# Optimization experiments

Measured on AMD Instinct MI355X. Metric: run time of the kernel, lower is better.

## Reference

```python
import jax, jax.numpy as jnp
import numpy as np

T = 16777216            # flat replay-buffer length (timesteps)
DISCOUNT = 0.99         # gamma
FINAL_REWARD = 0.0      # bootstrap value for the last timestep
TERM_PROB = 0.001       # ~1000-step episodes


def setup_inputs() -> dict:
    key = jax.random.key(0)
    k1, k2 = jax.random.split(key)
    reward = jax.random.normal(k1, (T,), dtype=jnp.float32)
    terminal = jax.random.bernoulli(k2, TERM_PROB, (T,))
    return {"terminal": terminal, "reward": reward}


def _discounted_cumret(terminal, reward):
    # Reverse-time linear recurrence (same math as tf.scan over reversed seq):
    #   c_t = r_t                      if terminal_t
    #   c_t = r_t + discount * c_{t+1} otherwise
    # i.e. c_t = a_t * c_{t+1} + b_t with a_t = discount*(1-term_t), b_t = r_t.
    # Expressed as a (log-depth) associative scan over the reversed sequence.
    a = jnp.where(terminal, jnp.zeros((), reward.dtype),
                  jnp.asarray(DISCOUNT, reward.dtype))
    a_rev = a[::-1]
    b_rev = reward[::-1]
    # fold the initializer (final_reward) into the first reversed element
    b_rev = b_rev.at[0].add(a_rev[0] * jnp.asarray(FINAL_REWARD, reward.dtype))

    def combine(e1, e2):
        # composition of affine maps x -> a*x + b (e1 applied first)
        a1, b1 = e1
        a2, b2 = e2
        return a1 * a2, a2 * b1 + b2

    _, y_rev = jax.lax.associative_scan(combine, (a_rev, b_rev))
    return y_rev[::-1]


def reference(terminal, reward):
    return _discounted_cumret(terminal, reward)
```

## Files before the change

### kernel.cpp

```cpp
#include <hip/hip_runtime.h>


constexpr int   TPB  = 256;
constexpr int   IPT  = 32;
constexpr int   TILE = TPB * IPT;
constexpr float DISC = 0.99f;
constexpr float L2DISC = -0.0144995696f;

__device__ __forceinline__ void wave_suffix_scan(float& A, float& B, int lane) {
    #pragma unroll
    for (int off = 1; off < 64; off <<= 1) {
        float oA = __shfl_down(A, off, 64);
        float oB = __shfl_down(B, off, 64);
        if (lane + off < 64) { B = A * oB + B; A = A * oA; }
    }
}

__global__ __launch_bounds__(TPB) void k_local(
        const int* __restrict__ term, const float* __restrict__ rew,
        float* __restrict__ out, float2* __restrict__ agg,
        int* __restrict__ lastT, long long T) {
    __shared__ float2 sWA[TPB / 64];
    __shared__ int    sLast[TPB / 64];

    const int t = threadIdx.x;
    const int lane = t & 63, wav = t >> 6;
    const int b = blockIdx.x;
    const long long lo   = (long long)b * TILE;
    const long long base = lo + (long long)t * IPT;
    const bool fast = (base + IPT <= T);

    float r[IPT];
    unsigned mask = 0;
    if (fast) {
        const float4* rp = (const float4*)(rew + base);
        const int4*   tp = (const int4*)(term + base);
        #pragma unroll
        for (int q = 0; q < IPT / 4; ++q) {
            float4 rv = rp[q];
            int4   tv = tp[q];
            r[4*q+0] = rv.x; r[4*q+1] = rv.y; r[4*q+2] = rv.z; r[4*q+3] = rv.w;
            mask |= (tv.x ? 1u : 0u) << (4*q+0);
            mask |= (tv.y ? 1u : 0u) << (4*q+1);
            mask |= (tv.z ? 1u : 0u) << (4*q+2);
            mask |= (tv.w ? 1u : 0u) << (4*q+3);
        }
    } else {
        #pragma unroll
        for (int k = 0; k < IPT; ++k) {
            long long i = base + k;
            if (i < T) { r[k] = rew[i]; mask |= (term[i] ? 1u : 0u) << k; }
            else       { r[k] = 0.f; }
        }
    }

    float A = 1.f, B = 0.f;
    #pragma unroll
    for (int k = IPT - 1; k >= 0; --k) {
        float ak = ((mask >> k) & 1u) ? 0.f : DISC;
        if (!fast && base + k >= T) ak = 1.f;
        B = ak * B + r[k]; A = ak * A;
    }

    float IA = A, IB = B;
    wave_suffix_scan(IA, IB, lane);

    int myLast = mask ? (int)(base + (31 - __clz(mask))) : -1;
    #pragma unroll
    for (int off = 32; off > 0; off >>= 1)
        myLast = max(myLast, __shfl_down(myLast, off, 64));

    if (lane == 0) { sWA[wav] = make_float2(IA, IB); sLast[wav] = myLast; }
    __syncthreads();

    if (t == 0) {
        float2 g = sWA[0];
        int lt = sLast[0];
        #pragma unroll
        for (int w = 1; w < TPB / 64; ++w) {
            float2 h = sWA[w];
            g.y = g.x * h.y + g.y; g.x = g.x * h.x;
            lt = max(lt, sLast[w]);
        }
        agg[b] = g;
        lastT[b] = max(lt, (int)lo - 1);
    }

    float EWA = 1.f, EWB = 0.f;
    #pragma unroll
    for (int w = 0; w < TPB / 64; ++w)
        if (w > wav) { float2 h = sWA[w]; EWB = EWA*h.y + EWB; EWA = EWA*h.x; }

    float EA = __shfl_down(IA, 1, 64);
    float EB = __shfl_down(IB, 1, 64);
    if (lane == 63) { EA = 1.f; EB = 0.f; }

    float y = EA * EWB + EB;

    #pragma unroll
    for (int k = IPT - 1; k >= 0; --k) {
        float ak = ((mask >> k) & 1u) ? 0.f : DISC;
        if (!fast && base + k >= T) ak = 1.f;
        y = ak * y + r[k]; r[k] = y;
    }

    if (fast) {
        float4* op = (float4*)(out + base);
        #pragma unroll
        for (int q = 0; q < IPT / 4; ++q)
            op[q] = make_float4(r[4*q+0], r[4*q+1], r[4*q+2], r[4*q+3]);
    } else {
        #pragma unroll
        for (int k = 0; k < IPT; ++k) {
            long long i = base + k;
            if (i < T) out[i] = r[k];
        }
    }
}

__global__ __launch_bounds__(TPB) void k_fix(
        const float2* __restrict__ agg, const int* __restrict__ lastT,
        float* __restrict__ out, int numBlocks, long long T) {
    __shared__ float2 sWB[TPB / 64];

    const int t = threadIdx.x;
    const int lane = t & 63, wav = t >> 6;
    const int b = blockIdx.x;

    const int cpt = (numBlocks + TPB - 1) / TPB;
    float VA = 1.f, VB = 0.f;
    #pragma unroll
    for (int k = cpt - 1; k >= 0; --k) {
        int g = t * cpt + k;
        if (g > b && g < numBlocks) {
            float2 q = agg[g];
            VB = q.x * VB + q.y; VA = q.x * VA;
        }
    }
    wave_suffix_scan(VA, VB, lane);
    if (lane == 0) sWB[wav] = make_float2(VA, VB);
    __syncthreads();

    float FA = sWB[0].x, FB = sWB[0].y;
    #pragma unroll
    for (int w = 1; w < TPB / 64; ++w) {
        float2 h = sWB[w];
        FB = FA * h.y + FB; FA = FA * h.x;
    }
    const float yin = FB;
    if (yin == 0.f) return;

    const long long lo = (long long)b * TILE;
    const long long hi = min(lo + TILE, T) - 1;
    const long long start = (long long)lastT[b] + 1;

    for (long long i = start + t; i <= hi; i += TPB) {
        float d = (float)(int)(hi + 1 - i);
        out[i] += exp2f(d * L2DISC) * yin;
    }
}

extern "C" void kernel_launch(void* const* d_in, const int* in_sizes, int n_in,
                              void* d_out, int out_size, void* d_ws, size_t ws_size,
                              hipStream_t stream) {
    const int*   term = (const int*)d_in[0];
    const float* rew  = (const float*)d_in[1];
    float*       out  = (float*)d_out;

    const long long T = (long long)in_sizes[1];
    const int numBlocks = (int)((T + TILE - 1) / TILE);

    float2* agg   = (float2*)d_ws;
    int*    lastT = (int*)(agg + numBlocks);

    k_local<<<numBlocks, TPB, 0, stream>>>(term, rew, out, agg, lastT, T);
    k_fix  <<<numBlocks, TPB, 0, stream>>>(agg, lastT, out, numBlocks, T);
}
```

Measured before the change: 183.3 us.

## Split block tile into register-prefetched chunks scanned back-to-front with carry

Each thread now handles four chunks of 8 elements instead of one run of 32. The block walks the chunks from last to first, carrying the running affine aggregate between them, and double-buffers the next chunk's loads in registers. The goal is to cut per-thread register use (32 floats down to 8) and get coalesced, chunk-contiguous memory access while overlapping loads with the scan. The cost is four block-wide scans and two barriers per chunk where there used to be one scan per tile.

After: 178.6 us. -2.6%, faster.

```diff
diff --git a/kernel.cpp b/kernel.cpp
--- a/kernel.cpp
+++ b/kernel.cpp
@@ -1,10 +1,12 @@
 #include <hip/hip_runtime.h>
 
 
-constexpr int   TPB  = 256;
-constexpr int   IPT  = 32;
-constexpr int   TILE = TPB * IPT;
-constexpr float DISC = 0.99f;
+constexpr int   TPB   = 256;
+constexpr int   IPTC  = 8;
+constexpr int   NCH   = 4;
+constexpr int   CHUNK = TPB * IPTC;
+constexpr int   TILE  = CHUNK * NCH;
+constexpr float DISC  = 0.99f;
 constexpr float L2DISC = -0.0144995696f;
 
 __device__ __forceinline__ void wave_suffix_scan(float& A, float& B, int lane) {
@@ -26,95 +28,182 @@
     const int t = threadIdx.x;
     const int lane = t & 63, wav = t >> 6;
     const int b = blockIdx.x;
-    const long long lo   = (long long)b * TILE;
-    const long long base = lo + (long long)t * IPT;
-    const bool fast = (base + IPT <= T);
-
-    float r[IPT];
-    unsigned mask = 0;
-    if (fast) {
-        const float4* rp = (const float4*)(rew + base);
-        const int4*   tp = (const int4*)(term + base);
+    const long long lo = (long long)b * TILE;
+    const bool fastblk = (lo + TILE <= T);
+
+    float At = 1.f, Bt = 0.f;
+    int   lt = -1;
+
+    if (fastblk) {
+        float4 bR[2][IPTC / 4];
+        int4   bT[2][IPTC / 4];
+
+        {
+            const long long base = lo + (long long)(NCH - 1) * CHUNK
+                                      + (long long)t * IPTC;
+            const float4* rp = (const float4*)(rew + base);
+            const int4*   tp = (const int4*)(term + base);
+            #pragma unroll
+            for (int q = 0; q < IPTC / 4; ++q) {
+                bR[(NCH - 1) & 1][q] = rp[q];
+                bT[(NCH - 1) & 1][q] = tp[q];
+            }
+        }
+
         #pragma unroll
-        for (int q = 0; q < IPT / 4; ++q) {
-            float4 rv = rp[q];
-            int4   tv = tp[q];
-            r[4*q+0] = rv.x; r[4*q+1] = rv.y; r[4*q+2] = rv.z; r[4*q+3] = rv.w;
-            mask |= (tv.x ? 1u : 0u) << (4*q+0);
-            mask |= (tv.y ? 1u : 0u) << (4*q+1);
-            mask |= (tv.z ? 1u : 0u) << (4*q+2);
-            mask |= (tv.w ? 1u : 0u) << (4*q+3);
+        for (int c = NCH - 1; c >= 0; --c) {
+            if (c > 0) {
+                const long long nbase = lo + (long long)(c - 1) * CHUNK
+                                           + (long long)t * IPTC;
+                const float4* rp = (const float4*)(rew + nbase);
+                const int4*   tp = (const int4*)(term + nbase);
+                #pragma unroll
+                for (int q = 0; q < IPTC / 4; ++q) {
+                    bR[(c - 1) & 1][q] = rp[q];
+                    bT[(c - 1) & 1][q] = tp[q];
+                }
+            }
+            const int p = c & 1;
+            const long long base = lo + (long long)c * CHUNK + (long long)t * IPTC;
+
+            float r[IPTC];
+            unsigned mask = 0;
+            #pragma unroll
+            for (int q = 0; q < IPTC / 4; ++q) {
+                float4 rv = bR[p][q];
+                int4   tv = bT[p][q];
+                r[4*q+0] = rv.x; r[4*q+1] = rv.y; r[4*q+2] = rv.z; r[4*q+3] = rv.w;
+                mask |= (tv.x ? 1u : 0u) << (4*q+0);
+                mask |= (tv.y ? 1u : 0u) << (4*q+1);
+                mask |= (tv.z ? 1u : 0u) << (4*q+2);
+                mask |= (tv.w ? 1u : 0u) << (4*q+3);
+            }
+
+            float A = 1.f, B = 0.f;
+            #pragma unroll
+            for (int k = IPTC - 1; k >= 0; --k) {
+                float ak = ((mask >> k) & 1u) ? 0.f : DISC;
+                B = ak * B + r[k]; A = ak * A;
+            }
+
+            float IA = A, IB = B;
+            wave_suffix_scan(IA, IB, lane);
+
+            int myLast = mask ? (int)(base + (31 - __clz(mask))) : -1;
+            #pragma unroll
+            for (int off = 32; off > 0; off >>= 1)
+                myLast = max(myLast, __shfl_down(myLast, off, 64));
+
+            if (lane == 0) { sWA[wav] = make_float2(IA, IB); sLast[wav] = myLast; }
+            __syncthreads();
+
+            float2 g = sWA[0];
+            int cl = sLast[0];
+            #pragma unroll
+            for (int w = 1; w < TPB / 64; ++w) {
+                float2 h = sWA[w];
+                g.y = g.x * h.y + g.y; g.x = g.x * h.x;
+                cl = max(cl, sLast[w]);
+            }
+            float EWA = 1.f, EWB = 0.f;
+            #pragma unroll
+            for (int w = 0; w < TPB / 64; ++w)
+                if (w > wav) { float2 h = sWA[w]; EWB = EWA*h.y + EWB; EWA = EWA*h.x; }
+
+            float EA = __shfl_down(IA, 1, 64);
+            float EB = __shfl_down(IB, 1, 64);
+            if (lane == 63) { EA = 1.f; EB = 0.f; }
+
+            const float Yc = Bt;
+            float y = EA * (EWA * Yc + EWB) + EB;
+
+            #pragma unroll
+            for (int k = IPTC - 1; k >= 0; --k) {
+                float ak = ((mask >> k) & 1u) ? 0.f : DISC;
+                y = ak * y + r[k]; r[k] = y;
+            }
+
+            float4* op = (float4*)(out + base);
+            #pragma unroll
+            for (int q = 0; q < IPTC / 4; ++q)
+                op[q] = make_float4(r[4*q+0], r[4*q+1], r[4*q+2], r[4*q+3]);
+
+            Bt = g.x * Bt + g.y;
+            At = g.x * At;
+            lt = max(lt, cl);
+            __syncthreads();
         }
     } else {
-        #pragma unroll
-        for (int k = 0; k < IPT; ++k) {
-            long long i = base + k;
-            if (i < T) { r[k] = rew[i]; mask |= (term[i] ? 1u : 0u) << k; }
-            else       { r[k] = 0.f; }
-        }
-    }
-
-    float A = 1.f, B = 0.f;
-    #pragma unroll
-    for (int k = IPT - 1; k >= 0; --k) {
-        float ak = ((mask >> k) & 1u) ? 0.f : DISC;
-        if (!fast && base + k >= T) ak = 1.f;
-        B = ak * B + r[k]; A = ak * A;
-    }
-
-    float IA = A, IB = B;
-    wave_suffix_scan(IA, IB, lane);
-
-    int myLast = mask ? (int)(base + (31 - __clz(mask))) : -1;
-    #pragma unroll
-    for (int off = 32; off > 0; off >>= 1)
-        myLast = max(myLast, __shfl_down(myLast, off, 64));
-
-    if (lane == 0) { sWA[wav] = make_float2(IA, IB); sLast[wav] = myLast; }
-    __syncthreads();
+        for (int c = NCH - 1; c >= 0; --c) {
+            const long long base = lo + (long long)c * CHUNK + (long long)t * IPTC;
+            float r[IPTC];
+            unsigned mask = 0;
+            #pragma unroll
+            for (int k = 0; k < IPTC; ++k) {
+                long long i = base + k;
+                if (i < T) { r[k] = rew[i]; mask |= (term[i] ? 1u : 0u) << k; }
+                else       { r[k] = 0.f; }
+            }
+            float A = 1.f, B = 0.f;
+            #pragma unroll
+            for (int k = IPTC - 1; k >= 0; --k) {
+                float ak = ((mask >> k) & 1u) ? 0.f : DISC;
+                if (base + k >= T) ak = 1.f;
+                B = ak * B + r[k]; A = ak * A;
+            }
+            float IA = A, IB = B;
+            wave_suffix_scan(IA, IB, lane);
+
+            int myLast = mask ? (int)(base + (31 - __clz(mask))) : -1;
+            #pragma unroll
+            for (int off = 32; off > 0; off >>= 1)
+                myLast = max(myLast, __shfl_down(myLast, off, 64));
+
+            if (lane == 0) { sWA[wav] = make_float2(IA, IB); sLast[wav] = myLast; }
+            __syncthreads();
+
+            float2 g = sWA[0];
+            int cl = sLast[0];
+            #pragma unroll
+            for (int w = 1; w < TPB / 64; ++w) {
+                float2 h = sWA[w];
+                g.y = g.x * h.y + g.y; g.x = g.x * h.x;
+                cl = max(cl, sLast[w]);
+            }
+            float EWA = 1.f, EWB = 0.f;
+            #pragma unroll
+            for (int w = 0; w < TPB / 64; ++w)
+                if (w > wav) { float2 h = sWA[w]; EWB = EWA*h.y + EWB; EWA = EWA*h.x; }
+
+            float EA = __shfl_down(IA, 1, 64);
+            float EB = __shfl_down(IB, 1, 64);
+            if (lane == 63) { EA = 1.f; EB = 0.f; }
+
+            const float Yc = Bt;
+            float y = EA * (EWA * Yc + EWB) + EB;
+
+            #pragma unroll
+            for (int k = IPTC - 1; k >= 0; --k) {
+                float ak = ((mask >> k) & 1u) ? 0.f : DISC;
+                if (base + k >= T) ak = 1.f;
+                y = ak * y + r[k]; r[k] = y;
+            }
+            #pragma unroll
+            for (int k = 0; k < IPTC; ++k) {
+                long long i = base + k;
+                if (i < T) out[i] = r[k];
+            }
+
+            Bt = g.x * Bt + g.y;
+            At = g.x * At;
+            lt = max(lt, cl);
+            __syncthreads();
+        }
+    }
 
     if (t == 0) {
-        float2 g = sWA[0];
-        int lt = sLast[0];
-        #pragma unroll
-        for (int w = 1; w < TPB / 64; ++w) {
-            float2 h = sWA[w];
-            g.y = g.x * h.y + g.y; g.x = g.x * h.x;
-            lt = max(lt, sLast[w]);
-        }
-        agg[b] = g;
+        agg[b] = make_float2(At, Bt);
         lastT[b] = max(lt, (int)lo - 1);
-    }
-
-    float EWA = 1.f, EWB = 0.f;
-    #pragma unroll
-    for (int w = 0; w < TPB / 64; ++w)
-        if (w > wav) { float2 h = sWA[w]; EWB = EWA*h.y + EWB; EWA = EWA*h.x; }
-
-    float EA = __shfl_down(IA, 1, 64);
-    float EB = __shfl_down(IB, 1, 64);
-    if (lane == 63) { EA = 1.f; EB = 0.f; }
-
-    float y = EA * EWB + EB;
-
-    #pragma unroll
-    for (int k = IPT - 1; k >= 0; --k) {
-        float ak = ((mask >> k) & 1u) ? 0.f : DISC;
-        if (!fast && base + k >= T) ak = 1.f;
-        y = ak * y + r[k]; r[k] = y;
-    }
-
-    if (fast) {
-        float4* op = (float4*)(out + base);
-        #pragma unroll
-        for (int q = 0; q < IPT / 4; ++q)
-            op[q] = make_float4(r[4*q+0], r[4*q+1], r[4*q+2], r[4*q+3]);
-    } else {
-        #pragma unroll
-        for (int k = 0; k < IPT; ++k) {
-            long long i = base + k;
-            if (i < T) out[i] = r[k];
-        }
     }
 }
 
```
